# Optimization experiments

Hardware: AMD Instinct MI355X
Metric: run time of the kernel (lower is better)

The kernel has to match this reference:

```python
import jax, jax.numpy as jnp
import numpy as np

B = 2
NUM_POINT = 1024   # sparse neural points
UP = 8             # up_ratio: samples per neural point
N_GEN = NUM_POINT * UP
N_DENSE = 8192
W_CD = 1.0; W_REG = 1.0; W_ARAP = 1.0; W_OVERLAP = 1.0


def _sqrdis(p, q):
    # p: [B,N,3], q: [B,M,3] -> [B,N,M] squared euclidean distances
    pn = jnp.sum(p * p, axis=-1)
    qn = jnp.sum(q * q, axis=-1)
    return pn[:, :, None] + qn[:, None, :] - 2.0 * jnp.einsum('bnd,bmd->bnm', p, q)


def _knn_idx(v, k):
    # torch_tensor_functions.get_neighbor_index: k nearest neighbors excluding self
    d = _sqrdis(v, v)
    _, idx = jax.lax.top_k(-d, k + 1)   # smallest distances
    return idx[:, :, 1:]


def _gather(t, idx):
    # t: [G,N,D], idx: [G,M,K] -> [G,M,K,D]
    return t[jnp.arange(t.shape[0])[:, None, None], idx]


def setup_inputs() -> dict:
    key = jax.random.key(0)
    ks = jax.random.split(key, 7)
    pts = lambda k, n: jax.random.normal(k, (B, n, 3), jnp.float32)
    return {
        'gen_points_batch': pts(ks[0], N_GEN),
        'gen_normals_batch': pts(ks[1], N_GEN),
        'uv_sampling_coors': jax.random.uniform(ks[2], (B, N_GEN, 2), jnp.float32),
        'train_points_sparse_batch': pts(ks[3], NUM_POINT),
        'train_normals_sparse_batch': pts(ks[4], NUM_POINT),
        'train_points_dense_batch': pts(ks[5], N_DENSE),
        'train_normals_dense_batch': pts(ks[6], N_DENSE),
        'num_point': NUM_POINT,
    }


def reference(gen_points_batch, gen_normals_batch, uv_sampling_coors,
              train_points_sparse_batch, train_normals_sparse_batch,
              train_points_dense_batch, train_normals_dense_batch, num_point):
    bs = gen_points_batch.shape[0]

    # ---- loss_on_cd (ChamferDistance = squared-dist nearest-neighbor both ways) ----
    d = _sqrdis(gen_points_batch, train_points_dense_batch)   # [B, N_GEN, N_DENSE]
    loss_cd = 0.5 * (jnp.sum(jnp.min(d, axis=-1)) + jnp.sum(jnp.min(d, axis=1))) / bs

    # ---- loss_on_reg ----
    up = gen_points_batch.shape[1] // train_points_sparse_batch.shape[1]
    g = gen_points_batch.reshape(bs, -1, up, 3)
    s = train_points_sparse_batch.reshape(bs, -1, 1, 3)
    squdis = jnp.sum((s - g) ** 2, axis=-1, keepdims=True)
    sign = jnp.sign(jax.lax.stop_gradient(squdis) - 0.04) * 0.5 + 1.0
    loss_reg = jnp.sum(squdis * sign) / bs

    # ---- loss_on_arap ----
    g_ = gen_points_batch.reshape(bs * num_point, -1, 3)
    uv = jax.lax.stop_gradient(uv_sampling_coors.reshape(bs * num_point, -1, 2))
    uv3 = jnp.concatenate([uv, jnp.zeros_like(uv[:, :, :1])], axis=-1)
    nidx = _knn_idx(uv3, 4)                                   # [B*P, up, 4]
    uv_nb = _gather(uv3, nidx)
    g_nb = _gather(g_, nidx)
    uv_d = jnp.sqrt(jnp.sum((uv_nb - uv3[:, :, None]) ** 2, axis=-1) + 1e-8)
    g_d = jnp.sqrt(jnp.sum((g_nb - g_[:, :, None]) ** 2, axis=-1) + 1e-8)
    scale = jax.lax.stop_gradient(jnp.sum(g_d)) / jnp.sum(uv_d)
    delta = uv_d * scale - g_d
    loss_arap = jnp.sum(delta * delta) / bs

    # ---- loss_on_overlap ----
    sp_idx = _knn_idx(train_points_sparse_batch, 6)           # [B, P, 6]
    sp_nb = _gather(train_points_sparse_batch, sp_idx).reshape(bs * num_point, -1, 3)
    g2 = gen_points_batch.reshape(bs * num_point, -1, 3)
    cross = _sqrdis(sp_nb, g2)                                # [B*P, 6, up]
    loss_overlap = jnp.sum(jnp.min(cross, axis=-1)) / bs

    return loss_cd * W_CD + loss_reg * W_REG + loss_arap * W_ARAP + loss_overlap * W_OVERLAP
```

## Files before the change

kernel.cpp:

```cpp
#include <hip/hip_runtime.h>

#define NB 2
#define NP 1024
#define UP 8
#define NG 8192
#define ND 8192

#define CD_CC 32
#define CD_CHUNK 256
#define CD_Q 8
#define CD_QB 2048
#define NCD 512
#define NRA 64
#define NOV (NB * NP / 4)

#define WS_MINS(ws)  ((unsigned int*)(ws))
#define WS_OV(ws)    ((double*)((char*)(ws) + (128 << 10)))
#define WS_RA(ws)    ((double*)((char*)(ws) + (132 << 10)))

typedef float v2f __attribute__((ext_vector_type(2)));
union F4 { float4 f; v2f h[2]; };

__device__ __forceinline__ v2f pk_fma(v2f a, v2f b, v2f c) {
  v2f d;
  asm("v_pk_fma_f32 %0, %1, %2, %3" : "=v"(d) : "v"(a), "v"(b), "v"(c));
  return d;
}

__device__ __forceinline__ float wave_reduce_sum(float v) {
  #pragma unroll
  for (int o = 32; o; o >>= 1) v += __shfl_down(v, o);
  return v;
}

__global__ __launch_bounds__(256) void mega_kernel(const float* __restrict__ gen,
                                                   const float* __restrict__ uv,
                                                   const float* __restrict__ sparse,
                                                   const float* __restrict__ dense,
                                                   void* __restrict__ ws) {
  __shared__ float4 shbuf[1024];
  __shared__ double aux[32];
  int blk = blockIdx.x;
  int tid = threadIdx.x;

  if (blk < NCD) {
    int qg = blk & 15;
    int chunk = blk >> 4;
    int dir = qg >> 3, b = (qg >> 2) & 1, qsub = qg & 3;
    const float* q; const float* t; unsigned int* mout;
    unsigned int* mins = WS_MINS(ws);
    if (dir == 0) { q = gen + (size_t)b * NG * 3;  t = dense + (size_t)b * ND * 3; mout = mins + b * NG; }
    else          { q = dense + (size_t)b * ND * 3; t = gen + (size_t)b * NG * 3;  mout = mins + NB * NG + b * ND; }

    {
      int gi = chunk * CD_CHUNK + tid;
      float tx = t[gi * 3 + 0], ty = t[gi * 3 + 1], tz = t[gi * 3 + 2];
      float tw = fmaf(tx, tx, fmaf(ty, ty, tz * tz));
      float sx = __shfl_xor(tx, 1), sy = __shfl_xor(ty, 1);
      float sz = __shfl_xor(tz, 1), sw = __shfl_xor(tw, 1);
      int P = tid >> 1;
      if (!(tid & 1)) shbuf[P]       = make_float4(tx, sx, ty, sy);
      else            shbuf[128 + P] = make_float4(sz, tz, sw, tw);
    }

    v2f ax2[CD_Q], ay2[CD_Q], az2[CD_Q];
    float qn[CD_Q], m[CD_Q];
    #pragma unroll
    for (int qq = 0; qq < CD_Q; ++qq) {
      int qi = qsub * CD_QB + qq * 256 + tid;
      float qx = q[qi * 3 + 0], qy = q[qi * 3 + 1], qz = q[qi * 3 + 2];
      qn[qq] = fmaf(qx, qx, fmaf(qy, qy, qz * qz));
      float ax = -2.f * qx, ay = -2.f * qy, az = -2.f * qz;
      ax2[qq] = (v2f){ax, ax}; ay2[qq] = (v2f){ay, ay}; az2[qq] = (v2f){az, az};
      m[qq] = 3.4e38f;
    }
    __syncthreads();

    #pragma unroll 2
    for (int j = 0; j < 128; ++j) {
      F4 uxy, uzw;
      uxy.f = shbuf[j];
      uzw.f = shbuf[128 + j];
      v2f X = uxy.h[0], Y = uxy.h[1], Z = uzw.h[0], W = uzw.h[1];
      #pragma unroll
      for (int qq = 0; qq < CD_Q; ++qq) {
        v2f d = pk_fma(az2[qq], Z, W);
        d = pk_fma(ay2[qq], Y, d);
        d = pk_fma(ax2[qq], X, d);
        m[qq] = fminf(fminf(m[qq], d.x), d.y);
      }
    }
    #pragma unroll
    for (int qq = 0; qq < CD_Q; ++qq) {
      int qi = qsub * CD_QB + qq * 256 + tid;
      atomicMin(&mout[qi], __float_as_uint(m[qq] + qn[qq]));
    }

  } else if (blk < NCD + NRA) {
    int lblk = blk - NCD;
    int id = lblk * 256 + tid;
    int gi = id >> 3, i = id & 7;
    const float* u = uv + (size_t)gi * UP * 2;
    const float* g = gen + (size_t)gi * UP * 3;
    float uxi = u[i * 2], uyi = u[i * 2 + 1];
    float gxi = g[i * 3], gyi = g[i * 3 + 1], gzi = g[i * 3 + 2];

    int b = gi >> 10, p = gi & (NP - 1);
    const float* s = sparse + ((size_t)b * NP + p) * 3;
    float rx = s[0] - gxi, ry = s[1] - gyi, rz = s[2] - gzi;
    float sq = rx * rx + ry * ry + rz * rz;
    float tt = sq - 0.04f;
    float reg = sq * (tt > 0.f ? 1.5f : (tt < 0.f ? 0.5f : 1.0f));

    float d2[UP], gd2[UP];
    #pragma unroll
    for (int j = 0; j < UP; ++j) {
      float dx = uxi - u[j * 2], dy = uyi - u[j * 2 + 1];
      d2[j] = dx * dx + dy * dy;
      float ex = gxi - g[j * 3], ey = gyi - g[j * 3 + 1], ez = gzi - g[j * 3 + 2];
      gd2[j] = ex * ex + ey * ey + ez * ez;
    }
    float suv = 0.f, sg = 0.f, suv2 = 0.f, sg2 = 0.f, suvg = 0.f;
    unsigned mask = 1u << i;
    #pragma unroll
    for (int k = 0; k < 4; ++k) {
      float bd = 3.4e38f, bg = 0.f; int bj = 0;
      #pragma unroll
      for (int j = 0; j < UP; ++j) {
        bool skip = (mask & (1u << j)) != 0;
        bool take = !skip && (d2[j] < bd);
        bd = take ? d2[j] : bd;
        bg = take ? gd2[j] : bg;
        bj = take ? j : bj;
      }
      mask |= 1u << bj;
      float uvd = sqrtf(bd + 1e-8f);
      float gd = sqrtf(bg + 1e-8f);
      suv += uvd; sg += gd;
      suv2 += uvd * uvd; sg2 += gd * gd; suvg += uvd * gd;
    }
    float v0 = wave_reduce_sum(reg), v1 = wave_reduce_sum(suv), v2 = wave_reduce_sum(sg);
    float v3 = wave_reduce_sum(suv2), v4 = wave_reduce_sum(sg2), v5 = wave_reduce_sum(suvg);
    int wave = tid >> 6;
    if ((tid & 63) == 0) {
      aux[wave * 6 + 0] = (double)v0; aux[wave * 6 + 1] = (double)v1;
      aux[wave * 6 + 2] = (double)v2; aux[wave * 6 + 3] = (double)v3;
      aux[wave * 6 + 4] = (double)v4; aux[wave * 6 + 5] = (double)v5;
    }
    __syncthreads();
    if (tid < 6) {
      double t6 = aux[tid] + aux[6 + tid] + aux[12 + tid] + aux[18 + tid];
      WS_RA(ws)[lblk * 6 + tid] = t6;
    }

  } else {
    int lblk = blk - NCD - NRA;
    int wave = tid >> 6, lane = tid & 63;
    int q = lblk * 4 + wave;
    int b = q >> 10, p = q & (NP - 1);
    const float* s = sparse + (size_t)b * NP * 3;
    for (int k = tid; k < NP; k += 256)
      shbuf[k] = make_float4(s[k * 3], s[k * 3 + 1], s[k * 3 + 2], 0.f);
    __syncthreads();

    float4 me = shbuf[p];
    float kd[7]; int ki[7];
    #pragma unroll
    for (int k = 0; k < 7; ++k) { kd[k] = 3.4e38f; ki[k] = 0; }
    #pragma unroll
    for (int jj = 0; jj < NP / 64; ++jj) {
      int j = jj * 64 + lane;
      float4 o = shbuf[j];
      float dx = me.x - o.x, dy = me.y - o.y, dz = me.z - o.z;
      float cd = fmaf(dx, dx, fmaf(dy, dy, dz * dz)); int cj = j;
      #pragma unroll
      for (int k = 0; k < 7; ++k) {
        bool sw = cd < kd[k];
        float td = sw ? kd[k] : cd;  int tj = sw ? ki[k] : cj;
        kd[k] = sw ? cd : kd[k];     ki[k] = sw ? cj : ki[k];
        cd = td; cj = tj;
      }
    }
    int nbr[6];
    unsigned long long key = ((unsigned long long)__float_as_uint(kd[0]) << 32) | (unsigned)ki[0];
    #pragma unroll
    for (int t = 0; t < 7; ++t) {
      unsigned long long mm = key;
      #pragma unroll
      for (int o = 32; o; o >>= 1) {
        unsigned long long other = __shfl_xor(mm, o);
        mm = other < mm ? other : mm;
      }
      if (t) nbr[t - 1] = (int)(unsigned)(mm & 0xffffffffu);
      bool win = (key == mm);
      #pragma unroll
      for (int k = 0; k < 6; ++k) { kd[k] = win ? kd[k + 1] : kd[k]; ki[k] = win ? ki[k + 1] : ki[k]; }
      if (win) kd[6] = 3.4e38f;
      key = ((unsigned long long)__float_as_uint(kd[0]) << 32) | (unsigned)ki[0];
    }

    float mval = 3.4e38f;
    if (lane < 48) {
      int n = lane >> 3, k = lane & 7;
      float4 o = shbuf[nbr[n]];
      const float* g = gen + ((size_t)b * NG + (size_t)p * UP + k) * 3;
      float dx = o.x - g[0], dy = o.y - g[1], dz = o.z - g[2];
      mval = fmaf(dx, dx, fmaf(dy, dy, dz * dz));
    }
    #pragma unroll
    for (int o = 1; o < 8; o <<= 1) mval = fminf(mval, __shfl_xor(mval, o));
    float ssum = 0.f;
    #pragma unroll
    for (int n = 0; n < 6; ++n) ssum += __shfl(mval, n * 8);

    if (lane == 0) aux[wave] = (double)ssum;
    __syncthreads();
    if (tid == 0) WS_OV(ws)[lblk] = aux[0] + aux[1] + aux[2] + aux[3];
  }
}

__global__ __launch_bounds__(1024) void final_kernel(void* __restrict__ ws, float* out) {
  __shared__ double red[16][9];
  int tid = threadIdx.x, wave = tid >> 6, lane = tid & 63;
  unsigned int* mins = WS_MINS(ws);
  const double* ov = WS_OV(ws);
  const double* ra = WS_RA(ws);
  const uint4* m4 = (const uint4*)mins;

  double s[9];
  #pragma unroll
  for (int k = 0; k < 9; ++k) s[k] = 0.0;
  #pragma unroll
  for (int i = 0; i < 4; ++i) {
    uint4 a = m4[tid + i * 1024];
    uint4 c = m4[tid + i * 1024 + 4096];
    s[0] += (double)__uint_as_float(a.x) + (double)__uint_as_float(a.y)
          + (double)__uint_as_float(a.z) + (double)__uint_as_float(a.w);
    s[1] += (double)__uint_as_float(c.x) + (double)__uint_as_float(c.y)
          + (double)__uint_as_float(c.z) + (double)__uint_as_float(c.w);
  }
  if (tid < NRA) {
    #pragma unroll
    for (int k = 0; k < 6; ++k) s[2 + k] = ra[tid * 6 + k];
  }
  if (tid < NOV) s[8] = ov[tid];

  #pragma unroll
  for (int k = 0; k < 9; ++k) {
    #pragma unroll
    for (int o = 32; o; o >>= 1) s[k] += __shfl_down(s[k], o);
  }
  if (lane == 0) {
    #pragma unroll
    for (int k = 0; k < 9; ++k) red[wave][k] = s[k];
  }
  __syncthreads();

  uint4* mw = (uint4*)mins;
  #pragma unroll
  for (int i = 0; i < 8; ++i)
    mw[tid + i * 1024] = make_uint4(0x7F800000u, 0x7F800000u, 0x7F800000u, 0x7F800000u);

  if (tid == 0) {
    double t[9];
    #pragma unroll
    for (int k = 0; k < 9; ++k) {
      t[k] = 0.0;
      for (int w = 0; w < 16; ++w) t[k] += red[w][k];
    }
    double loss_cd = 0.5 * (t[0] + t[1]) / NB;
    double loss_reg = t[2] / NB;
    double scale = t[4] / t[3];
    double loss_arap = (scale * scale * t[5] + t[6] - 2.0 * scale * t[7]) / NB;
    double loss_ov = t[8] / NB;
    out[0] = (float)(loss_cd + loss_reg + loss_arap + loss_ov);
  }
}

extern "C" void kernel_launch(void* const* d_in, const int* in_sizes, int n_in,
                              void* d_out, int out_size, void* d_ws, size_t ws_size,
                              hipStream_t stream) {
  const float* gen    = (const float*)d_in[0];
  const float* uvc    = (const float*)d_in[2];
  const float* sparse = (const float*)d_in[3];
  const float* dense  = (const float*)d_in[5];
  float* out = (float*)d_out;

  mega_kernel<<<NCD + NRA + NOV, 256, 0, stream>>>(gen, uvc, sparse, dense, d_ws);
  final_kernel<<<1, 1024, 0, stream>>>(d_ws, out);
}
```

Baseline: 36.07 us.

## Fuse reduction into cooperative kernel with grid syncs and rebalance Chamfer blocks

Merges the main loss kernel and the final reduction into one cooperative launch. Grid-wide syncs separate a parallel partial-reduction phase from a single-thread finalisation, which removes the second kernel launch and the single-block tail. The Chamfer work is split into twice as many blocks, each handling 4 queries instead of 8, and each overlap block now handles 2 points instead of 1. A plain two-kernel fallback is kept for when occupancy cannot fit all blocks at once. The cost is two grid barriers plus host-side occupancy and device-attribute queries on every launch.

```diff
diff --git a/kernel.cpp b/kernel.cpp
--- a/kernel.cpp
+++ b/kernel.cpp
@@ -1,4 +1,7 @@
 #include <hip/hip_runtime.h>
+#include <hip/hip_cooperative_groups.h>
+
+namespace cg = cooperative_groups;
 
 #define NB 2
 #define NP 1024
@@ -6,17 +9,15 @@
 #define NG 8192
 #define ND 8192
 
-#define CD_CC 32
-#define CD_CHUNK 256
-#define CD_Q 8
-#define CD_QB 2048
-#define NCD 512
+#define NCD 1024
 #define NRA 64
-#define NOV (NB * NP / 4)
+#define NOV 256
+#define NTOT (NCD + NRA + NOV)
 
 #define WS_MINS(ws)  ((unsigned int*)(ws))
 #define WS_OV(ws)    ((double*)((char*)(ws) + (128 << 10)))
 #define WS_RA(ws)    ((double*)((char*)(ws) + (132 << 10)))
+#define WS_FIN(ws)   ((double*)((char*)(ws) + (136 << 10)))
 
 typedef float v2f __attribute__((ext_vector_type(2)));
 union F4 { float4 f; v2f h[2]; };
@@ -32,28 +33,30 @@
   for (int o = 32; o; o >>= 1) v += __shfl_down(v, o);
   return v;
 }
-
-__global__ __launch_bounds__(256) void mega_kernel(const float* __restrict__ gen,
-                                                   const float* __restrict__ uv,
-                                                   const float* __restrict__ sparse,
-                                                   const float* __restrict__ dense,
-                                                   void* __restrict__ ws) {
-  __shared__ float4 shbuf[1024];
-  __shared__ double aux[32];
-  int blk = blockIdx.x;
-  int tid = threadIdx.x;
-
+__device__ __forceinline__ double wave_reduce_sum_d(double v) {
+  #pragma unroll
+  for (int o = 32; o; o >>= 1) v += __shfl_down(v, o);
+  return v;
+}
+
+__device__ __forceinline__ void phaseA(int blk, int tid,
+                                       const float* __restrict__ gen,
+                                       const float* __restrict__ uv,
+                                       const float* __restrict__ sparse,
+                                       const float* __restrict__ dense,
+                                       void* __restrict__ ws,
+                                       float4* shbuf, double* aux) {
   if (blk < NCD) {
-    int qg = blk & 15;
-    int chunk = blk >> 4;
-    int dir = qg >> 3, b = (qg >> 2) & 1, qsub = qg & 3;
+    int qg = blk & 31;
+    int chunk = blk >> 5;
+    int dir = qg >> 4, b = (qg >> 3) & 1, qsub = qg & 7;
     const float* q; const float* t; unsigned int* mout;
     unsigned int* mins = WS_MINS(ws);
     if (dir == 0) { q = gen + (size_t)b * NG * 3;  t = dense + (size_t)b * ND * 3; mout = mins + b * NG; }
     else          { q = dense + (size_t)b * ND * 3; t = gen + (size_t)b * NG * 3;  mout = mins + NB * NG + b * ND; }
 
     {
-      int gi = chunk * CD_CHUNK + tid;
+      int gi = chunk * 256 + tid;
       float tx = t[gi * 3 + 0], ty = t[gi * 3 + 1], tz = t[gi * 3 + 2];
       float tw = fmaf(tx, tx, fmaf(ty, ty, tz * tz));
       float sx = __shfl_xor(tx, 1), sy = __shfl_xor(ty, 1);
@@ -63,11 +66,11 @@
       else            shbuf[128 + P] = make_float4(sz, tz, sw, tw);
     }
 
-    v2f ax2[CD_Q], ay2[CD_Q], az2[CD_Q];
-    float qn[CD_Q], m[CD_Q];
-    #pragma unroll
-    for (int qq = 0; qq < CD_Q; ++qq) {
-      int qi = qsub * CD_QB + qq * 256 + tid;
+    v2f ax2[4], ay2[4], az2[4];
+    float qn[4], m[4];
+    #pragma unroll
+    for (int qq = 0; qq < 4; ++qq) {
+      int qi = qsub * 1024 + qq * 256 + tid;
       float qx = q[qi * 3 + 0], qy = q[qi * 3 + 1], qz = q[qi * 3 + 2];
       qn[qq] = fmaf(qx, qx, fmaf(qy, qy, qz * qz));
       float ax = -2.f * qx, ay = -2.f * qy, az = -2.f * qz;
@@ -76,14 +79,14 @@
     }
     __syncthreads();
 
-    #pragma unroll 2
+    #pragma unroll 4
     for (int j = 0; j < 128; ++j) {
       F4 uxy, uzw;
       uxy.f = shbuf[j];
       uzw.f = shbuf[128 + j];
       v2f X = uxy.h[0], Y = uxy.h[1], Z = uzw.h[0], W = uzw.h[1];
       #pragma unroll
-      for (int qq = 0; qq < CD_Q; ++qq) {
+      for (int qq = 0; qq < 4; ++qq) {
         v2f d = pk_fma(az2[qq], Z, W);
         d = pk_fma(ay2[qq], Y, d);
         d = pk_fma(ax2[qq], X, d);
@@ -91,8 +94,8 @@
       }
     }
     #pragma unroll
-    for (int qq = 0; qq < CD_Q; ++qq) {
-      int qi = qsub * CD_QB + qq * 256 + tid;
+    for (int qq = 0; qq < 4; ++qq) {
+      int qi = qsub * 1024 + qq * 256 + tid;
       atomicMin(&mout[qi], __float_as_uint(m[qq] + qn[qq]));
     }
 
@@ -156,67 +159,152 @@
   } else {
     int lblk = blk - NCD - NRA;
     int wave = tid >> 6, lane = tid & 63;
-    int q = lblk * 4 + wave;
-    int b = q >> 10, p = q & (NP - 1);
+    int qbase = lblk * 8 + wave * 2;
+    int b = qbase >> 10;
     const float* s = sparse + (size_t)b * NP * 3;
     for (int k = tid; k < NP; k += 256)
       shbuf[k] = make_float4(s[k * 3], s[k * 3 + 1], s[k * 3 + 2], 0.f);
     __syncthreads();
 
-    float4 me = shbuf[p];
-    float kd[7]; int ki[7];
-    #pragma unroll
-    for (int k = 0; k < 7; ++k) { kd[k] = 3.4e38f; ki[k] = 0; }
-    #pragma unroll
-    for (int jj = 0; jj < NP / 64; ++jj) {
-      int j = jj * 64 + lane;
-      float4 o = shbuf[j];
-      float dx = me.x - o.x, dy = me.y - o.y, dz = me.z - o.z;
-      float cd = fmaf(dx, dx, fmaf(dy, dy, dz * dz)); int cj = j;
-      #pragma unroll
-      for (int k = 0; k < 7; ++k) {
-        bool sw = cd < kd[k];
-        float td = sw ? kd[k] : cd;  int tj = sw ? ki[k] : cj;
-        kd[k] = sw ? cd : kd[k];     ki[k] = sw ? cj : ki[k];
-        cd = td; cj = tj;
-      }
-    }
-    int nbr[6];
-    unsigned long long key = ((unsigned long long)__float_as_uint(kd[0]) << 32) | (unsigned)ki[0];
-    #pragma unroll
-    for (int t = 0; t < 7; ++t) {
-      unsigned long long mm = key;
-      #pragma unroll
-      for (int o = 32; o; o >>= 1) {
-        unsigned long long other = __shfl_xor(mm, o);
-        mm = other < mm ? other : mm;
-      }
-      if (t) nbr[t - 1] = (int)(unsigned)(mm & 0xffffffffu);
-      bool win = (key == mm);
-      #pragma unroll
-      for (int k = 0; k < 6; ++k) { kd[k] = win ? kd[k + 1] : kd[k]; ki[k] = win ? ki[k + 1] : ki[k]; }
-      if (win) kd[6] = 3.4e38f;
-      key = ((unsigned long long)__float_as_uint(kd[0]) << 32) | (unsigned)ki[0];
-    }
-
-    float mval = 3.4e38f;
-    if (lane < 48) {
-      int n = lane >> 3, k = lane & 7;
-      float4 o = shbuf[nbr[n]];
-      const float* g = gen + ((size_t)b * NG + (size_t)p * UP + k) * 3;
-      float dx = o.x - g[0], dy = o.y - g[1], dz = o.z - g[2];
-      mval = fmaf(dx, dx, fmaf(dy, dy, dz * dz));
-    }
-    #pragma unroll
-    for (int o = 1; o < 8; o <<= 1) mval = fminf(mval, __shfl_xor(mval, o));
-    float ssum = 0.f;
-    #pragma unroll
-    for (int n = 0; n < 6; ++n) ssum += __shfl(mval, n * 8);
-
-    if (lane == 0) aux[wave] = (double)ssum;
+    float ssum_tot = 0.f;
+    for (int qq2 = 0; qq2 < 2; ++qq2) {
+      int q = qbase + qq2;
+      int p = q & (NP - 1);
+      float4 me = shbuf[p];
+      float kd[7]; int ki[7];
+      #pragma unroll
+      for (int k = 0; k < 7; ++k) { kd[k] = 3.4e38f; ki[k] = 0; }
+      #pragma unroll
+      for (int jj = 0; jj < NP / 64; ++jj) {
+        int j = jj * 64 + lane;
+        float4 o = shbuf[j];
+        float dx = me.x - o.x, dy = me.y - o.y, dz = me.z - o.z;
+        float cd = fmaf(dx, dx, fmaf(dy, dy, dz * dz)); int cj = j;
+        #pragma unroll
+        for (int k = 0; k < 7; ++k) {
+          bool sw = cd < kd[k];
+          float td = sw ? kd[k] : cd;  int tj = sw ? ki[k] : cj;
+          kd[k] = sw ? cd : kd[k];     ki[k] = sw ? cj : ki[k];
+          cd = td; cj = tj;
+        }
+      }
+      int nbr[6];
+      unsigned long long key = ((unsigned long long)__float_as_uint(kd[0]) << 32) | (unsigned)ki[0];
+      #pragma unroll
+      for (int t = 0; t < 7; ++t) {
+        unsigned long long mm = key;
+        #pragma unroll
+        for (int o = 32; o; o >>= 1) {
+          unsigned long long other = __shfl_xor(mm, o);
+          mm = other < mm ? other : mm;
+        }
+        if (t) nbr[t - 1] = (int)(unsigned)(mm & 0xffffffffu);
+        bool win = (key == mm);
+        #pragma unroll
+        for (int k = 0; k < 6; ++k) { kd[k] = win ? kd[k + 1] : kd[k]; ki[k] = win ? ki[k + 1] : ki[k]; }
+        if (win) kd[6] = 3.4e38f;
+        key = ((unsigned long long)__float_as_uint(kd[0]) << 32) | (unsigned)ki[0];
+      }
+
+      float mval = 3.4e38f;
+      if (lane < 48) {
+        int n = lane >> 3, k = lane & 7;
+        float4 o = shbuf[nbr[n]];
+        const float* g = gen + ((size_t)b * NG + (size_t)p * UP + k) * 3;
+        float dx = o.x - g[0], dy = o.y - g[1], dz = o.z - g[2];
+        mval = fmaf(dx, dx, fmaf(dy, dy, dz * dz));
+      }
+      #pragma unroll
+      for (int o = 1; o < 8; o <<= 1) mval = fminf(mval, __shfl_xor(mval, o));
+      #pragma unroll
+      for (int n = 0; n < 6; ++n) ssum_tot += __shfl(mval, n * 8);
+    }
+
+    if (lane == 0) aux[wave] = (double)ssum_tot;
     __syncthreads();
     if (tid == 0) WS_OV(ws)[lblk] = aux[0] + aux[1] + aux[2] + aux[3];
   }
+}
+
+__device__ __forceinline__ void phaseB(int blk, int tid, void* __restrict__ ws, double* aux) {
+  if (blk < 16) {
+    unsigned int* mu = WS_MINS(ws);
+    int base = blk * 2048 + tid;
+    double s = 0.0;
+    #pragma unroll
+    for (int j = 0; j < 8; ++j) {
+      unsigned v = __hip_atomic_load(&mu[base + j * 256], __ATOMIC_RELAXED, __HIP_MEMORY_SCOPE_AGENT);
+      s += (double)__uint_as_float(v);
+    }
+    s = wave_reduce_sum_d(s);
+    if ((tid & 63) == 0) aux[tid >> 6] = s;
+    __syncthreads();
+    if (tid == 0) WS_FIN(ws)[blk] = aux[0] + aux[1] + aux[2] + aux[3];
+    uint4* m4 = (uint4*)mu;
+    uint4 inf4 = make_uint4(0x7F800000u, 0x7F800000u, 0x7F800000u, 0x7F800000u);
+    m4[blk * 512 + tid] = inf4;
+    m4[blk * 512 + 256 + tid] = inf4;
+  } else if (blk == 16) {
+    double s = WS_OV(ws)[tid];
+    s = wave_reduce_sum_d(s);
+    if ((tid & 63) == 0) aux[tid >> 6] = s;
+    __syncthreads();
+    if (tid == 0) WS_FIN(ws)[16] = aux[0] + aux[1] + aux[2] + aux[3];
+  } else if (blk == 17) {
+    if (tid < 64) {
+      const double* ra = WS_RA(ws);
+      double s0 = ra[tid * 6 + 0], s1 = ra[tid * 6 + 1], s2 = ra[tid * 6 + 2];
+      double s3 = ra[tid * 6 + 3], s4 = ra[tid * 6 + 4], s5 = ra[tid * 6 + 5];
+      s0 = wave_reduce_sum_d(s0); s1 = wave_reduce_sum_d(s1); s2 = wave_reduce_sum_d(s2);
+      s3 = wave_reduce_sum_d(s3); s4 = wave_reduce_sum_d(s4); s5 = wave_reduce_sum_d(s5);
+      if (tid == 0) {
+        double* fin = WS_FIN(ws);
+        fin[17] = s0; fin[18] = s1; fin[19] = s2; fin[20] = s3; fin[21] = s4; fin[22] = s5;
+      }
+    }
+  }
+}
+
+__device__ __forceinline__ void phaseC(void* __restrict__ ws, float* out) {
+  double f[23];
+  #pragma unroll
+  for (int k = 0; k < 23; ++k)
+    f[k] = __hip_atomic_load(&WS_FIN(ws)[k], __ATOMIC_RELAXED, __HIP_MEMORY_SCOPE_AGENT);
+  double t0 = 0.0, t1 = 0.0;
+  #pragma unroll
+  for (int k = 0; k < 8; ++k) { t0 += f[k]; t1 += f[8 + k]; }
+  double loss_cd = 0.5 * (t0 + t1) / NB;
+  double loss_reg = f[17] / NB;
+  double scale = f[19] / f[18];
+  double loss_arap = (scale * scale * f[20] + f[21] - 2.0 * scale * f[22]) / NB;
+  double loss_ov = f[16] / NB;
+  out[0] = (float)(loss_cd + loss_reg + loss_arap + loss_ov);
+}
+
+__global__ __launch_bounds__(256, 6) void mega_coop(const float* __restrict__ gen,
+                                                    const float* __restrict__ uv,
+                                                    const float* __restrict__ sparse,
+                                                    const float* __restrict__ dense,
+                                                    void* __restrict__ ws,
+                                                    float* __restrict__ out) {
+  __shared__ float4 shbuf[1024];
+  __shared__ double aux[32];
+  int blk = blockIdx.x, tid = threadIdx.x;
+  phaseA(blk, tid, gen, uv, sparse, dense, ws, shbuf, aux);
+  cg::this_grid().sync();
+  phaseB(blk, tid, ws, aux);
+  cg::this_grid().sync();
+  if (blk == 0 && tid == 0) phaseC(ws, out);
+}
+
+__global__ __launch_bounds__(256) void mega_plain(const float* __restrict__ gen,
+                                                  const float* __restrict__ uv,
+                                                  const float* __restrict__ sparse,
+                                                  const float* __restrict__ dense,
+                                                  void* __restrict__ ws) {
+  __shared__ float4 shbuf[1024];
+  __shared__ double aux[32];
+  phaseA(blockIdx.x, threadIdx.x, gen, uv, sparse, dense, ws, shbuf, aux);
 }
 
 __global__ __launch_bounds__(1024) void final_kernel(void* __restrict__ ws, float* out) {
@@ -246,10 +334,7 @@
   if (tid < NOV) s[8] = ov[tid];
 
   #pragma unroll
-  for (int k = 0; k < 9; ++k) {
-    #pragma unroll
-    for (int o = 32; o; o >>= 1) s[k] += __shfl_down(s[k], o);
-  }
+  for (int k = 0; k < 9; ++k) s[k] = wave_reduce_sum_d(s[k]);
   if (lane == 0) {
     #pragma unroll
     for (int k = 0; k < 9; ++k) red[wave][k] = s[k];
@@ -257,9 +342,9 @@
   __syncthreads();
 
   uint4* mw = (uint4*)mins;
-  #pragma unroll
-  for (int i = 0; i < 8; ++i)
-    mw[tid + i * 1024] = make_uint4(0x7F800000u, 0x7F800000u, 0x7F800000u, 0x7F800000u);
+  uint4 inf4 = make_uint4(0x7F800000u, 0x7F800000u, 0x7F800000u, 0x7F800000u);
+  #pragma unroll
+  for (int i = 0; i < 8; ++i) mw[tid + i * 1024] = inf4;
 
   if (tid == 0) {
     double t[9];
@@ -286,6 +371,18 @@
   const float* dense  = (const float*)d_in[5];
   float* out = (float*)d_out;
 
-  mega_kernel<<<NCD + NRA + NOV, 256, 0, stream>>>(gen, uvc, sparse, dense, d_ws);
-  final_kernel<<<1, 1024, 0, stream>>>(d_ws, out);
-}
+  int nCU = 0, maxBlk = 0;
+  hipDeviceGetAttribute(&nCU, hipDeviceAttributeMultiprocessorCount, 0);
+  hipOccupancyMaxActiveBlocksPerMultiprocessor(&maxBlk, (const void*)mega_coop, 256, 0);
+
+  if ((long)maxBlk * nCU >= NTOT) {
+    void* ws_p = d_ws;
+    void* args[6] = {(void*)&gen, (void*)&uvc, (void*)&sparse, (void*)&dense,
+                     (void*)&ws_p, (void*)&out};
+    hipLaunchCooperativeKernel((const void*)mega_coop, dim3(NTOT), dim3(256),
+                               args, 0, stream);
+  } else {
+    mega_plain<<<NTOT, 256, 0, stream>>>(gen, uvc, sparse, dense, d_ws);
+    final_kernel<<<1, 1024, 0, stream>>>(d_ws, out);
+  }
+}
```

Result: slower. 39.69 us (+10.0%).
